# Performance work log

Hardware: AMD Instinct MI355X
Metric: run time of the kernel (lower is better)

Reference implementation:

```python
import jax, jax.numpy as jnp
import numpy as np

DIM = 256
HEADS = 8
DHEAD = 32          # dim // 8
WIN = 128           # attn_window
NBLOCKS = 4
FF_INNER = int(DIM * 4 * 2 / 3)  # 682
SCALE = DHEAD ** -0.5


def layernorm(x, g, b):
    mu = jnp.mean(x, axis=-1, keepdims=True)
    var = jnp.mean((x - mu) ** 2, axis=-1, keepdims=True)
    return (x - mu) * jax.lax.rsqrt(var + 1e-5) * g + b


def look_around(x):
    # x: (b, h, nw, w, d) -> (b, h, nw, 3w, d); prev/current/next window, zero-padded ends
    nw = x.shape[2]
    p = jnp.pad(x, ((0, 0), (0, 0), (1, 1), (0, 0), (0, 0)))
    return jnp.concatenate([p[:, :, i:i + nw] for i in range(3)], axis=3)


def key_mask(mask):
    # mask: (b, n) bool -> (b, nw, 3w) validity of look-around keys
    b, n = mask.shape
    nw = n // WIN
    mb = mask.reshape(b, nw, WIN)
    p = jnp.pad(mb, ((0, 0), (1, 1), (0, 0)), constant_values=False)
    return jnp.concatenate([p[:, i:i + nw] for i in range(3)], axis=-1)


def local_mha(x, kmask, ln_g, ln_b, qkv_w, out_w):
    b, n, _ = x.shape
    nw = n // WIN
    xn = layernorm(x, ln_g, ln_b)
    qkv = jnp.einsum('bnd,ed->bne', xn, qkv_w)           # (b, n, 3*h*dh)
    qkv = qkv.reshape(b, nw, WIN, 3, HEADS, DHEAD)
    q, k, v = [jnp.transpose(qkv[:, :, :, i], (0, 3, 1, 2, 4)) for i in range(3)]  # (b,h,nw,w,dh)
    kk = look_around(k)                                   # (b,h,nw,3w,dh)
    vv = look_around(v)
    sim = jnp.einsum('bhnid,bhnjd->bhnij', q, kk) * SCALE  # (b,h,nw,w,3w)
    neg = -jnp.finfo(sim.dtype).max
    sim = jnp.where(kmask[:, None, :, None, :], sim, neg)
    attn = jax.nn.softmax(sim, axis=-1)
    out = jnp.einsum('bhnij,bhnjd->bhnid', attn, vv)      # (b,h,nw,w,dh)
    out = jnp.transpose(out, (0, 2, 3, 1, 4)).reshape(b, n, HEADS * DHEAD)
    return jnp.einsum('bne,de->bnd', out, out_w)


def geglu_ff(x, ln_g, ln_b, w1, w2):
    xn = layernorm(x, ln_g, ln_b)
    h = jnp.einsum('bnd,ed->bne', xn, w1)                 # (b, n, 2*FF_INNER)
    a, g = jnp.split(h, 2, axis=-1)
    y = a * jax.nn.gelu(g, approximate=False)             # exact GELU like torch
    return jnp.einsum('bne,de->bnd', y, w2)


def setup_inputs() -> dict:
    key = jax.random.key(0)
    ks = jax.random.split(key, 8)
    B, N = 8, 4096
    s = 0.02
    return {
        'x': jax.random.normal(ks[0], (B, N, DIM), dtype=jnp.float32),
        'mask': jnp.ones((B, N), dtype=bool),
        'ln1_g': jnp.ones((NBLOCKS, DIM), jnp.float32),
        'ln1_b': jnp.zeros((NBLOCKS, DIM), jnp.float32),
        'qkv_w': jax.random.normal(ks[1], (NBLOCKS, 3 * HEADS * DHEAD, DIM), jnp.float32) * s,
        'out_w': jax.random.normal(ks[2], (NBLOCKS, DIM, HEADS * DHEAD), jnp.float32) * s,
        'ln2_g': jnp.ones((NBLOCKS, DIM), jnp.float32),
        'ln2_b': jnp.zeros((NBLOCKS, DIM), jnp.float32),
        'ff_w1': jax.random.normal(ks[3], (NBLOCKS, 2 * FF_INNER, DIM), jnp.float32) * s,
        'ff_w2': jax.random.normal(ks[4], (NBLOCKS, DIM, FF_INNER), jnp.float32) * s,
    }


def reference(x, mask, ln1_g, ln1_b, qkv_w, out_w, ln2_g, ln2_b, ff_w1, ff_w2):
    kmask = key_mask(mask)
    for i in range(NBLOCKS):
        x = local_mha(x, kmask, ln1_g[i], ln1_b[i], qkv_w[i], out_w[i]) + x
        x = geglu_ff(x, ln2_g[i], ln2_b[i], ff_w1[i], ff_w2[i]) + x
    return x
```

## Files before the change

### kernel.cpp

```cpp
#include <hip/hip_runtime.h>


#define DIM 256
#define DHEAD 32
#define NWIN 32
#define SEQ 4096
#define TOKENS 32768
#define FFP 704
#define ATT_SCALE_LOG2E 0.25501818642228136f

typedef __attribute__((ext_vector_type(4))) float f32x4;
typedef __attribute__((ext_vector_type(4))) short s16x4;
typedef __attribute__((ext_vector_type(8))) short s16x8;
typedef __attribute__((ext_vector_type(4))) _Float16 f16x4;
typedef __attribute__((ext_vector_type(8))) _Float16 f16x8;

__device__ __forceinline__ short f2bf(float f) {
  unsigned int u = __float_as_uint(f);
  u += 0x7fffu + ((u >> 16) & 1u);
  return (short)(u >> 16);
}

__device__ __forceinline__ float fast_exp2(float x) {
#if __has_builtin(__builtin_amdgcn_exp2f)
  return __builtin_amdgcn_exp2f(x);
#else
  return __expf(x * 0.6931471805599453f);
#endif
}

__device__ __forceinline__ float gelu_as(float g) {
  const float z = fabsf(g) * 0.70710678118654752440f;
#if __has_builtin(__builtin_amdgcn_rcpf)
  const float t = __builtin_amdgcn_rcpf(fmaf(0.3275911f, z, 1.0f));
#else
  const float t = 1.0f / fmaf(0.3275911f, z, 1.0f);
#endif
  const float e = fast_exp2(-z * z * 1.4426950408889634f);
  const float poly = t * fmaf(t, fmaf(t, fmaf(t, fmaf(t, 1.061405429f,
                     -1.453152027f), 1.421413741f), -0.284496736f), 0.254829592f);
  const float erfv = fmaf(-poly, e, 1.0f);
  const float se = (g < 0.0f) ? -erfv : erfv;
  return 0.5f * g * (1.0f + se);
}

__device__ __forceinline__ void gl_lds16(const short* g, short* l) {
  __builtin_amdgcn_global_load_lds(
      (const __attribute__((address_space(1))) void*)g,
      (__attribute__((address_space(3))) void*)l, 16, 0, 0);
}

__device__ __forceinline__ s16x8 fragld(const short* lds, int row, int g) {
  return *(const s16x8*)(lds + row * 64 + ((g ^ (row & 7)) << 3));
}

__global__ void __launch_bounds__(256)
copy_ln(const float* __restrict__ x0, const float* __restrict__ gw,
        const float* __restrict__ bw, float* __restrict__ x, short* __restrict__ xn) {
  const int row = blockIdx.x * 4 + (threadIdx.x >> 6);
  const int lane = threadIdx.x & 63;
  const f32x4 v = *(const f32x4*)(x0 + (size_t)row * DIM + lane * 4);
  *(f32x4*)(x + (size_t)row * DIM + lane * 4) = v;
  float s = v[0] + v[1] + v[2] + v[3];
  float s2 = v[0]*v[0] + v[1]*v[1] + v[2]*v[2] + v[3]*v[3];
#pragma unroll
  for (int off = 32; off > 0; off >>= 1) {
    s  += __shfl_xor(s, off, 64);
    s2 += __shfl_xor(s2, off, 64);
  }
  const float mu = s * (1.0f / DIM);
  const float var = s2 * (1.0f / DIM) - mu * mu;
  const float rstd = rsqrtf(var + 1e-5f);
  const f32x4 gv = *(const f32x4*)(gw + lane * 4);
  const f32x4 bv = *(const f32x4*)(bw + lane * 4);
  s16x4 o;
#pragma unroll
  for (int j = 0; j < 4; ++j) o[j] = f2bf((v[j] - mu) * rstd * gv[j] + bv[j]);
  *(s16x4*)(xn + (size_t)row * DIM + lane * 4) = o;
}

template<int K, bool DO_LN>
__global__ void __launch_bounds__(256, 2)
gemm_res_ln(const short* __restrict__ A, const short* __restrict__ W,
            float* __restrict__ x, const float* __restrict__ lng,
            const float* __restrict__ lnb, short* __restrict__ xn) {
  __shared__ short As[2][64 * 64];
  __shared__ short Bs[2][256 * 64];
  const int tid = threadIdx.x;
  const int lane = tid & 63;
  const int w = tid >> 6;
  const int ln16 = lane & 15;
  const int quad = lane >> 4;
  const int m_blk = blockIdx.x * 64;
  const int n0w = w * 64;
  const int srow = lane >> 3;
  const int swz = (lane & 7) ^ srow;

  const short* sg[10];
  short* dg0[10];
  short* dg1[10];
#pragma unroll
  for (int i = 0; i < 10; ++i) {
    const int grp = w + i * 4;
    if (grp < 8) {
      sg[i] = A + (size_t)(m_blk + grp * 8 + srow) * K + swz * 8;
      dg0[i] = &As[0][grp * 512];
      dg1[i] = &As[1][grp * 512];
    } else {
      const int gb = grp - 8;
      sg[i] = W + (size_t)(gb * 8 + srow) * K + swz * 8;
      dg0[i] = &Bs[0][gb * 512];
      dg1[i] = &Bs[1][gb * 512];
    }
  }

  constexpr int NS = K / 64;
  f32x4 acc[4][4] = {};

#pragma unroll
  for (int i = 0; i < 10; ++i) gl_lds16(sg[i], dg0[i]);
  __syncthreads();

#pragma unroll
  for (int s = 0; s < NS; ++s) {
    if (s + 1 < NS) {
#pragma unroll
      for (int i = 0; i < 10; ++i)
        gl_lds16(sg[i] + (s + 1) * 64, ((s & 1) ? dg0 : dg1)[i]);
    }
    const short* Ac = (s & 1) ? As[1] : As[0];
    const short* Bc = (s & 1) ? Bs[1] : Bs[0];
    s16x8 af[2][4], bf[2][4];
#pragma unroll
    for (int kh = 0; kh < 2; ++kh) {
#pragma unroll
      for (int mt = 0; mt < 4; ++mt)
        af[kh][mt] = fragld(Ac, mt * 16 + ln16, kh * 4 + quad);
#pragma unroll
      for (int nt = 0; nt < 4; ++nt)
        bf[kh][nt] = fragld(Bc, n0w + nt * 16 + ln16, kh * 4 + quad);
    }
#pragma unroll
    for (int kh = 0; kh < 2; ++kh)
#pragma unroll
      for (int mt = 0; mt < 4; ++mt)
#pragma unroll
        for (int nt = 0; nt < 4; ++nt)
          acc[mt][nt] = __builtin_amdgcn_mfma_f32_16x16x32_bf16(af[kh][mt], bf[kh][nt], acc[mt][nt], 0, 0, 0);
    __syncthreads();
  }

#pragma unroll
  for (int mt = 0; mt < 4; ++mt)
#pragma unroll
    for (int nt = 0; nt < 4; ++nt)
#pragma unroll
      for (int r = 0; r < 4; ++r) {
        const size_t idx = (size_t)(m_blk + mt * 16 + quad * 4 + r) * DIM
                           + n0w + nt * 16 + ln16;
        const float v = x[idx] + acc[mt][nt][r];
        acc[mt][nt][r] = v;
        x[idx] = v;
      }

  if (DO_LN) {
    float2* red = (float2*)As[0];
#pragma unroll
    for (int mt = 0; mt < 4; ++mt)
#pragma unroll
      for (int r = 0; r < 4; ++r) {
        float s = 0.f, s2 = 0.f;
#pragma unroll
        for (int nt = 0; nt < 4; ++nt) {
          const float v = acc[mt][nt][r];
          s += v; s2 += v * v;
        }
#pragma unroll
        for (int off = 1; off < 16; off <<= 1) {
          s  += __shfl_xor(s, off, 64);
          s2 += __shfl_xor(s2, off, 64);
        }
        if (ln16 == 0)
          red[(mt * 16 + quad * 4 + r) * 4 + w] = float2{s, s2};
      }
    __syncthreads();

    float gv[4], bv[4];
#pragma unroll
    for (int nt = 0; nt < 4; ++nt) {
      gv[nt] = lng[n0w + nt * 16 + ln16];
      bv[nt] = lnb[n0w + nt * 16 + ln16];
    }
#pragma unroll
    for (int mt = 0; mt < 4; ++mt)
#pragma unroll
      for (int r = 0; r < 4; ++r) {
        const int row = mt * 16 + quad * 4 + r;
        const float2 t0 = red[row * 4 + 0];
        const float2 t1 = red[row * 4 + 1];
        const float2 t2 = red[row * 4 + 2];
        const float2 t3 = red[row * 4 + 3];
        const float s  = (t0.x + t1.x) + (t2.x + t3.x);
        const float s2 = (t0.y + t1.y) + (t2.y + t3.y);
        const float mu = s * (1.0f / DIM);
        const float var = s2 * (1.0f / DIM) - mu * mu;
        const float rstd = rsqrtf(var + 1e-5f);
#pragma unroll
        for (int nt = 0; nt < 4; ++nt)
          xn[(size_t)(m_blk + row) * DIM + n0w + nt * 16 + ln16] =
              f2bf((acc[mt][nt][r] - mu) * rstd * gv[nt] + bv[nt]);
      }
  }
}

__global__ void __launch_bounds__(256, 2)
fused_out_ff1(const short* __restrict__ A, const short* __restrict__ W,
              float* __restrict__ x, const float* __restrict__ lng,
              const float* __restrict__ lnb, const short* __restrict__ wff,
              short* __restrict__ y) {
  __shared__ short As[2][64 * 64];
  __shared__ short Bs[2][256 * 64];
  const int tid = threadIdx.x;
  const int lane = tid & 63;
  const int w = tid >> 6;
  const int ln16 = lane & 15;
  const int quad = lane >> 4;
  const int m_blk = blockIdx.x * 64;
  const int n0w = w * 64;
  const int srow = lane >> 3;
  const int swz = (lane & 7) ^ srow;

  const short* sg[10];
  short* dg0[10];
  short* dg1[10];
#pragma unroll
  for (int i = 0; i < 10; ++i) {
    const int grp = w + i * 4;
    if (grp < 8) {
      sg[i] = A + (size_t)(m_blk + grp * 8 + srow) * DIM + swz * 8;
      dg0[i] = &As[0][grp * 512];
      dg1[i] = &As[1][grp * 512];
    } else {
      const int gb = grp - 8;
      sg[i] = W + (size_t)(gb * 8 + srow) * DIM + swz * 8;
      dg0[i] = &Bs[0][gb * 512];
      dg1[i] = &Bs[1][gb * 512];
    }
  }

  f32x4 acc[4][4] = {};
#pragma unroll
  for (int i = 0; i < 10; ++i) gl_lds16(sg[i], dg0[i]);
  __syncthreads();

#pragma unroll
  for (int s = 0; s < 4; ++s) {
    if (s + 1 < 4) {
#pragma unroll
      for (int i = 0; i < 10; ++i)
        gl_lds16(sg[i] + (s + 1) * 64, ((s & 1) ? dg0 : dg1)[i]);
    }
    const short* Ac = (s & 1) ? As[1] : As[0];
    const short* Bc = (s & 1) ? Bs[1] : Bs[0];
    s16x8 af[2][4], bf[2][4];
#pragma unroll
    for (int kh = 0; kh < 2; ++kh) {
#pragma unroll
      for (int mt = 0; mt < 4; ++mt)
        af[kh][mt] = fragld(Ac, mt * 16 + ln16, kh * 4 + quad);
#pragma unroll
      for (int nt = 0; nt < 4; ++nt)
        bf[kh][nt] = fragld(Bc, n0w + nt * 16 + ln16, kh * 4 + quad);
    }
#pragma unroll
    for (int kh = 0; kh < 2; ++kh)
#pragma unroll
      for (int mt = 0; mt < 4; ++mt)
#pragma unroll
        for (int nt = 0; nt < 4; ++nt)
          acc[mt][nt] = __builtin_amdgcn_mfma_f32_16x16x32_bf16(af[kh][mt], bf[kh][nt], acc[mt][nt], 0, 0, 0);
    __syncthreads();
  }

  short* const xnl = &Bs[0][0];
  short* const Wsl = &Bs[1][0];
  int wbase[4];
#pragma unroll
  for (int i = 0; i < 4; ++i) {
    const int grp = w + i * 4;
    const int half = grp >> 3;
    wbase[i] = (half * FFP + (grp & 7) * 8 + srow) * DIM + swz * 8;
  }
  auto stage2 = [&](int cs2) {
    const int c2 = cs2 >> 2, s2 = cs2 & 3;
    short* db = Wsl + ((cs2 & 1) ? 8192 : 0);
#pragma unroll
    for (int i = 0; i < 4; ++i)
      gl_lds16(wff + wbase[i] + c2 * (64 * DIM) + s2 * 64, db + (w + i * 4) * 512);
  };
  stage2(0);

#pragma unroll
  for (int mt = 0; mt < 4; ++mt)
#pragma unroll
    for (int nt = 0; nt < 4; ++nt)
#pragma unroll
      for (int r = 0; r < 4; ++r) {
        const size_t idx = (size_t)(m_blk + mt * 16 + quad * 4 + r) * DIM
                           + n0w + nt * 16 + ln16;
        const float v = x[idx] + acc[mt][nt][r];
        acc[mt][nt][r] = v;
        x[idx] = v;
      }

  {
    float2* red = (float2*)As[0];
#pragma unroll
    for (int mt = 0; mt < 4; ++mt)
#pragma unroll
      for (int r = 0; r < 4; ++r) {
        float s = 0.f, s2 = 0.f;
#pragma unroll
        for (int nt = 0; nt < 4; ++nt) {
          const float v = acc[mt][nt][r];
          s += v; s2 += v * v;
        }
#pragma unroll
        for (int off = 1; off < 16; off <<= 1) {
          s  += __shfl_xor(s, off, 64);
          s2 += __shfl_xor(s2, off, 64);
        }
        if (ln16 == 0)
          red[(mt * 16 + quad * 4 + r) * 4 + w] = float2{s, s2};
      }
    __syncthreads();

    float gv[4], bv[4];
#pragma unroll
    for (int nt = 0; nt < 4; ++nt) {
      gv[nt] = lng[n0w + nt * 16 + ln16];
      bv[nt] = lnb[n0w + nt * 16 + ln16];
    }
#pragma unroll
    for (int mt = 0; mt < 4; ++mt)
#pragma unroll
      for (int r = 0; r < 4; ++r) {
        const int row = mt * 16 + quad * 4 + r;
        const float2 t0 = red[row * 4 + 0];
        const float2 t1 = red[row * 4 + 1];
        const float2 t2 = red[row * 4 + 2];
        const float2 t3 = red[row * 4 + 3];
        const float s  = (t0.x + t1.x) + (t2.x + t3.x);
        const float s2 = (t0.y + t1.y) + (t2.y + t3.y);
        const float mu = s * (1.0f / DIM);
        const float var = s2 * (1.0f / DIM) - mu * mu;
        const float rstd = rsqrtf(var + 1e-5f);
#pragma unroll
        for (int nt = 0; nt < 4; ++nt) {
          const int colin = nt * 16 + ln16;
          const int pos = ((colin >> 3) ^ (row & 7)) * 8 + (colin & 7);
          xnl[w * 4096 + row * 64 + pos] =
              f2bf((acc[mt][nt][r] - mu) * rstd * gv[nt] + bv[nt]);
        }
      }
  }
  __syncthreads();

  f32x4 aA[4], aG[4];
  for (int cs = 0; cs < 44; ++cs) {
    const int c = cs >> 2, s = cs & 3;
    if (cs + 1 < 44) stage2(cs + 1);
    if (s == 0) {
#pragma unroll
      for (int mt = 0; mt < 4; ++mt) { aA[mt] = f32x4{0.f,0.f,0.f,0.f}; aG[mt] = f32x4{0.f,0.f,0.f,0.f}; }
    }
    const short* Wb = Wsl + ((cs & 1) ? 8192 : 0);
    const short* Xs = xnl + s * 4096;
    s16x8 af[2][4], wa[2], wg[2];
#pragma unroll
    for (int kh = 0; kh < 2; ++kh) {
#pragma unroll
      for (int mt = 0; mt < 4; ++mt)
        af[kh][mt] = fragld(Xs, mt * 16 + ln16, kh * 4 + quad);
      wa[kh] = fragld(Wb, w * 16 + ln16, kh * 4 + quad);
      wg[kh] = fragld(Wb, 64 + w * 16 + ln16, kh * 4 + quad);
    }
#pragma unroll
    for (int kh = 0; kh < 2; ++kh)
#pragma unroll
      for (int mt = 0; mt < 4; ++mt) {
        aA[mt] = __builtin_amdgcn_mfma_f32_16x16x32_bf16(af[kh][mt], wa[kh], aA[mt], 0, 0, 0);
        aG[mt] = __builtin_amdgcn_mfma_f32_16x16x32_bf16(af[kh][mt], wg[kh], aG[mt], 0, 0, 0);
      }
    if (s == 3) {
      const int col = c * 64 + w * 16 + ln16;
#pragma unroll
      for (int mt = 0; mt < 4; ++mt)
#pragma unroll
        for (int r = 0; r < 4; ++r)
          y[(size_t)(m_blk + mt * 16 + quad * 4 + r) * FFP + col] =
              f2bf(aA[mt][r] * gelu_as(aG[mt][r]));
    }
    __syncthreads();
  }
}

__global__ void __launch_bounds__(256)
gemm_qkv(const short* __restrict__ A, const short* __restrict__ W,
         short* __restrict__ qh, short* __restrict__ kh_, _Float16* __restrict__ vp) {
  __shared__ short As[128 * 64];
  __shared__ short Bs[128 * 64];
  const int tid = threadIdx.x;
  const int lane = tid & 63;
  const int w = tid >> 6;
  const int ln16 = lane & 15;
  const int quad = lane >> 4;
  const int m_blk0 = blockIdx.x * 256;
  const int n_blk = blockIdx.y * 128;
  const int m0w = (w & 1) * 64;
  const int n0w = (w >> 1) * 64;
  const int srow = lane >> 3;
  const int swz = (lane & 7) ^ srow;

  int aoff[4];
  const short* bsrc[4];
  short* dst[8];
#pragma unroll
  for (int i = 0; i < 8; ++i) {
    const int grp = w + i * 4;
    if (i < 4) {
      aoff[i] = (grp * 8 + srow) * DIM + swz * 8;
      dst[i] = As + grp * 512;
    } else {
      const int gb = grp - 16;
      bsrc[i - 4] = W + (size_t)(n_blk + gb * 8 + srow) * DIM + swz * 8;
      dst[i] = Bs + gb * 512;
    }
  }

  auto stage = [&](int t2, int s2) {
    const short* At = A + (size_t)(m_blk0 + t2 * 128) * DIM + s2 * 64;
#pragma unroll
    for (int i = 0; i < 4; ++i) gl_lds16(At + aoff[i], dst[i]);
#pragma unroll
    for (int i = 0; i < 4; ++i) gl_lds16(bsrc[i] + s2 * 64, dst[i + 4]);
  };

  stage(0, 0);

#pragma unroll
  for (int t = 0; t < 2; ++t) {
    f32x4 acc[4][4] = {};
#pragma unroll
    for (int s = 0; s < 4; ++s) {
      __syncthreads();
      s16x8 af[2][4], bf[2][4];
#pragma unroll
      for (int kh = 0; kh < 2; ++kh) {
#pragma unroll
        for (int mt = 0; mt < 4; ++mt)
          af[kh][mt] = fragld(As, m0w + mt * 16 + ln16, kh * 4 + quad);
#pragma unroll
        for (int nt = 0; nt < 4; ++nt)
          bf[kh][nt] = fragld(Bs, n0w + nt * 16 + ln16, kh * 4 + quad);
      }
#pragma unroll
      for (int kh = 0; kh < 2; ++kh)
#pragma unroll
        for (int mt = 0; mt < 4; ++mt)
#pragma unroll
          for (int nt = 0; nt < 4; ++nt)
            acc[mt][nt] = __builtin_amdgcn_mfma_f32_16x16x32_bf16(af[kh][mt], bf[kh][nt], acc[mt][nt], 0, 0, 0);
      if (!(t == 1 && s == 3)) {
        __syncthreads();
        if (s == 3) stage(t + 1, 0);
        else        stage(t, s + 1);
      }
    }

#pragma unroll
    for (int mt = 0; mt < 4; ++mt) {
      const int m = m_blk0 + t * 128 + m0w + mt * 16 + quad * 4;
      const int bb = m >> 12;
      const int n = m & 4095;
#pragma unroll
      for (int nt = 0; nt < 4; ++nt) {
        const int f = n_blk + n0w + nt * 16;
        if (f < 512) {
          const int ff = f & 255;
          short* dstp = (f < 256 ? qh : kh_)
                       + ((size_t)(bb * 8 + (ff >> 5)) * SEQ + n) * 32 + (ff & 16) + ln16;
#pragma unroll
          for (int r = 0; r < 4; ++r) dstp[r * 32] = f2bf(acc[mt][nt][r]);
        } else {
          const int ff = f - 512;
          const int h = ff >> 5;
          const int d = (ff & 16) + ln16;
          const int within = n & 31;
          const int pos = (n & ~31) + ((within & 12) << 1) + ((within >> 4) << 2);
          f16x4 o;
#pragma unroll
          for (int r = 0; r < 4; ++r) o[r] = (_Float16)acc[mt][nt][r];
          *(f16x4*)(vp + ((size_t)(bb * 8 + h) * 32 + d) * SEQ + pos) = o;
        }
      }
    }
  }
}

__global__ void __launch_bounds__(256)
attn_kernel(const short* __restrict__ qh, const short* __restrict__ kh,
            const _Float16* __restrict__ vp, short* __restrict__ out) {
  const int blk = blockIdx.x;
  const int lane = threadIdx.x & 63;
  const int wid = threadIdx.x >> 6;
  const int ln16 = lane & 15;
  const int quad = lane >> 4;

  const int w = (blk & 15) * 2 + (wid >> 1);
  const int h = (blk >> 4) & 7;
  const int b = blk >> 7;
  const int plane = b * 8 + h;
  const int tok0 = w * 128 + (wid & 1) * 64;
  const int ktok = w * 128 - 128;
  const int c0 = (w == 0) ? 4 : 0;
  const int c1 = (w == NWIN - 1) ? 8 : 12;

  const short* qp = qh + ((size_t)plane * SEQ + tok0) * 32;
  s16x8 qf[4];
#pragma unroll
  for (int qi = 0; qi < 4; ++qi)
    qf[qi] = *(const s16x8*)(qp + (qi * 16 + ln16) * 32 + quad * 8);

  const short* kp = kh + ((size_t)plane * SEQ + ktok) * 32;
  const _Float16* vb = vp + ((size_t)plane * 32 + ln16) * SEQ + ktok;

  float lsum[4] = {0.f, 0.f, 0.f, 0.f};
  f32x4 ot[4][2] = {};

  s16x8 kc0 = *(const s16x8*)(kp + (c0 * 32 + ln16) * 32 + quad * 8);
  s16x8 kc1 = *(const s16x8*)(kp + (c0 * 32 + 16 + ln16) * 32 + quad * 8);
  f16x8 vc0 = *(const f16x8*)(vb + c0 * 32 + quad * 8);
  f16x8 vc1 = *(const f16x8*)(vb + (size_t)16 * SEQ + c0 * 32 + quad * 8);

  for (int c = c0; c < c1; ++c) {
    const int cn = (c + 1 < c1) ? c + 1 : c;
    s16x8 kn0 = *(const s16x8*)(kp + (cn * 32 + ln16) * 32 + quad * 8);
    s16x8 kn1 = *(const s16x8*)(kp + (cn * 32 + 16 + ln16) * 32 + quad * 8);
    f16x8 vn0 = *(const f16x8*)(vb + cn * 32 + quad * 8);
    f16x8 vn1 = *(const f16x8*)(vb + (size_t)16 * SEQ + cn * 32 + quad * 8);

    const f16x4 v00 = __builtin_shufflevector(vc0, vc0, 0, 1, 2, 3);
    const f16x4 v10 = __builtin_shufflevector(vc0, vc0, 4, 5, 6, 7);
    const f16x4 v01 = __builtin_shufflevector(vc1, vc1, 0, 1, 2, 3);
    const f16x4 v11 = __builtin_shufflevector(vc1, vc1, 4, 5, 6, 7);

#pragma unroll
    for (int qi = 0; qi < 4; ++qi) {
      const f32x4 z = {0.f, 0.f, 0.f, 0.f};
      f32x4 st0 = __builtin_amdgcn_mfma_f32_16x16x32_bf16(kc0, qf[qi], z, 0, 0, 0);
      f32x4 st1 = __builtin_amdgcn_mfma_f32_16x16x32_bf16(kc1, qf[qi], z, 0, 0, 0);
      float p[8];
#pragma unroll
      for (int r = 0; r < 4; ++r) {
        p[r]     = fast_exp2(st0[r] * ATT_SCALE_LOG2E);
        p[4 + r] = fast_exp2(st1[r] * ATT_SCALE_LOG2E);
      }
      lsum[qi] += ((p[0] + p[1]) + (p[2] + p[3])) + ((p[4] + p[5]) + (p[6] + p[7]));
      f16x4 pa, pb;
#pragma unroll
      for (int r = 0; r < 4; ++r) { pa[r] = (_Float16)p[r]; pb[r] = (_Float16)p[4 + r]; }
      ot[qi][0] = __builtin_amdgcn_mfma_f32_16x16x16f16(pa, v00, ot[qi][0], 0, 0, 0);
      ot[qi][1] = __builtin_amdgcn_mfma_f32_16x16x16f16(pa, v01, ot[qi][1], 0, 0, 0);
      ot[qi][0] = __builtin_amdgcn_mfma_f32_16x16x16f16(pb, v10, ot[qi][0], 0, 0, 0);
      ot[qi][1] = __builtin_amdgcn_mfma_f32_16x16x16f16(pb, v11, ot[qi][1], 0, 0, 0);
    }
    kc0 = kn0; kc1 = kn1; vc0 = vn0; vc1 = vn1;
  }

#pragma unroll
  for (int qi = 0; qi < 4; ++qi) {
    float l = lsum[qi];
    l += __shfl_xor(l, 16, 64);
    l += __shfl_xor(l, 32, 64);
    const float inv = 1.0f / l;
#pragma unroll
    for (int dt = 0; dt < 2; ++dt)
#pragma unroll
      for (int r = 0; r < 4; ++r)
        out[(size_t)(b * SEQ + tok0 + qi * 16 + quad * 4 + r) * DIM
            + h * DHEAD + dt * 16 + ln16] = f2bf(ot[qi][dt][r] * inv);
  }
}

__global__ void cvt_all(const float* __restrict__ qkv_w, const float* __restrict__ out_w,
                        const float* __restrict__ ff_w1, const float* __restrict__ ff_w2,
                        short* __restrict__ wqkv, short* __restrict__ wout,
                        short* __restrict__ wff1, short* __restrict__ wff2) {
  int i = blockIdx.x * 256 + threadIdx.x;
  if (i < 786432) { wqkv[i] = f2bf(qkv_w[i]); return; }
  i -= 786432;
  if (i < 262144) { wout[i] = f2bf(out_w[i]); return; }
  i -= 262144;
  if (i < 1441792) {
    const int c = i & 255;
    const int rl = i >> 8;
    const int l = rl / 1408;
    const int r = rl - l * 1408;
    const int half = r / FFP;
    const int rr = r - half * FFP;
    const float v = (rr < 682) ? ff_w1[((size_t)(l * 1364 + half * 682 + rr)) * 256 + c] : 0.0f;
    wff1[i] = f2bf(v);
    return;
  }
  i -= 1441792;
  if (i < 720896) {
    const int c = i % FFP;
    const int t = i / FFP;
    const float v = (c < 682) ? ff_w2[(size_t)t * 682 + c] : 0.0f;
    wff2[i] = f2bf(v);
  }
}

extern "C" void kernel_launch(void* const* d_in, const int* in_sizes, int n_in,
                              void* d_out, int out_size, void* d_ws, size_t ws_size,
                              hipStream_t stream) {
  const float* x0    = (const float*)d_in[0];
  const float* ln1_g = (const float*)d_in[2];
  const float* ln1_b = (const float*)d_in[3];
  const float* qkv_w = (const float*)d_in[4];
  const float* out_w = (const float*)d_in[5];
  const float* ln2_g = (const float*)d_in[6];
  const float* ln2_b = (const float*)d_in[7];
  const float* ff_w1 = (const float*)d_in[8];
  const float* ff_w2 = (const float*)d_in[9];
  float* x = (float*)d_out;

  char* ws = (char*)d_ws;
  short* wqkv = (short*)(ws);
  short* wout = (short*)(ws + 1572864);
  short* wff1 = (short*)(ws + 2097152);
  short* wff2 = (short*)(ws + 4980736);
  short* xn   = (short*)(ws + 6422528);
  short*    qhb = (short*)(ws + 23199744);
  short*    khb = (short*)(ws + 23199744 + 16777216);
  _Float16* vpb = (_Float16*)(ws + 23199744 + 33554432);
  short*    yb  = (short*)(ws + 23199744);

  copy_ln<<<8192, 256, 0, stream>>>(x0, ln1_g, ln1_b, x, xn);
  cvt_all<<<12544, 256, 0, stream>>>(qkv_w, out_w, ff_w1, ff_w2, wqkv, wout, wff1, wff2);

  for (int l = 0; l < 4; ++l) {
    gemm_qkv<<<dim3(128, 6), 256, 0, stream>>>(
        xn, wqkv + (size_t)l * 768 * DIM, qhb, khb, vpb);
    attn_kernel<<<1024, 256, 0, stream>>>(qhb, khb, vpb, xn);
    fused_out_ff1<<<512, 256, 0, stream>>>(
        xn, wout + (size_t)l * DIM * DIM, x,
        ln2_g + l * DIM, ln2_b + l * DIM,
        wff1 + (size_t)l * 2 * FFP * DIM, yb);
    if (l < 3)
      gemm_res_ln<FFP, true><<<512, 256, 0, stream>>>(
          yb, wff2 + (size_t)l * DIM * FFP, x,
          ln1_g + (l + 1) * DIM, ln1_b + (l + 1) * DIM, xn);
    else
      gemm_res_ln<FFP, false><<<512, 256, 0, stream>>>(
          yb, wff2 + (size_t)l * DIM * FFP, x, nullptr, nullptr, nullptr);
  }
}
```

Measured before the change: 718.6 us.

## Load weight fragments directly from global memory instead of staging through LDS

In gemm_res_ln and fused_out_ff1, the B (weight) operand is no longer copied into shared memory. Each lane now reads its MFMA fragments straight from global memory, relying on L1/L2 caching because every block reuses the same small weight matrix. The FF1 loop also drops its LDS double-buffered weight staging and the per-chunk barriers, and the 2-blocks-per-CU launch bound is removed. This frees a lot of LDS and removes sync overhead, at the cost of uncoalesced global loads on the critical path whose latency is no longer hidden by a prefetch.

```diff
diff --git a/kernel.cpp b/kernel.cpp
--- a/kernel.cpp
+++ b/kernel.cpp
@@ -80,12 +80,11 @@
 }
 
 template<int K, bool DO_LN>
-__global__ void __launch_bounds__(256, 2)
+__global__ void __launch_bounds__(256)
 gemm_res_ln(const short* __restrict__ A, const short* __restrict__ W,
             float* __restrict__ x, const float* __restrict__ lng,
             const float* __restrict__ lnb, short* __restrict__ xn) {
   __shared__ short As[2][64 * 64];
-  __shared__ short Bs[2][256 * 64];
   const int tid = threadIdx.x;
   const int lane = tid & 63;
   const int w = tid >> 6;
@@ -96,50 +95,48 @@
   const int srow = lane >> 3;
   const int swz = (lane & 7) ^ srow;
 
-  const short* sg[10];
-  short* dg0[10];
-  short* dg1[10];
-#pragma unroll
-  for (int i = 0; i < 10; ++i) {
+  const short* sg[2];
+  short* dg0[2];
+  short* dg1[2];
+#pragma unroll
+  for (int i = 0; i < 2; ++i) {
     const int grp = w + i * 4;
-    if (grp < 8) {
-      sg[i] = A + (size_t)(m_blk + grp * 8 + srow) * K + swz * 8;
-      dg0[i] = &As[0][grp * 512];
-      dg1[i] = &As[1][grp * 512];
-    } else {
-      const int gb = grp - 8;
-      sg[i] = W + (size_t)(gb * 8 + srow) * K + swz * 8;
-      dg0[i] = &Bs[0][gb * 512];
-      dg1[i] = &Bs[1][gb * 512];
-    }
-  }
+    sg[i] = A + (size_t)(m_blk + grp * 8 + srow) * K + swz * 8;
+    dg0[i] = &As[0][grp * 512];
+    dg1[i] = &As[1][grp * 512];
+  }
+
+  const short* wr[4];
+#pragma unroll
+  for (int nt = 0; nt < 4; ++nt)
+    wr[nt] = W + (size_t)(n0w + nt * 16 + ln16) * K + quad * 8;
 
   constexpr int NS = K / 64;
   f32x4 acc[4][4] = {};
 
 #pragma unroll
-  for (int i = 0; i < 10; ++i) gl_lds16(sg[i], dg0[i]);
+  for (int i = 0; i < 2; ++i) gl_lds16(sg[i], dg0[i]);
   __syncthreads();
 
 #pragma unroll
   for (int s = 0; s < NS; ++s) {
     if (s + 1 < NS) {
 #pragma unroll
-      for (int i = 0; i < 10; ++i)
+      for (int i = 0; i < 2; ++i)
         gl_lds16(sg[i] + (s + 1) * 64, ((s & 1) ? dg0 : dg1)[i]);
     }
     const short* Ac = (s & 1) ? As[1] : As[0];
-    const short* Bc = (s & 1) ? Bs[1] : Bs[0];
     s16x8 af[2][4], bf[2][4];
 #pragma unroll
-    for (int kh = 0; kh < 2; ++kh) {
+    for (int nt = 0; nt < 4; ++nt) {
+      bf[0][nt] = *(const s16x8*)(wr[nt] + s * 64);
+      bf[1][nt] = *(const s16x8*)(wr[nt] + s * 64 + 32);
+    }
+#pragma unroll
+    for (int kh = 0; kh < 2; ++kh)
 #pragma unroll
       for (int mt = 0; mt < 4; ++mt)
         af[kh][mt] = fragld(Ac, mt * 16 + ln16, kh * 4 + quad);
-#pragma unroll
-      for (int nt = 0; nt < 4; ++nt)
-        bf[kh][nt] = fragld(Bc, n0w + nt * 16 + ln16, kh * 4 + quad);
-    }
 #pragma unroll
     for (int kh = 0; kh < 2; ++kh)
 #pragma unroll
@@ -213,13 +210,13 @@
   }
 }
 
-__global__ void __launch_bounds__(256, 2)
+__global__ void __launch_bounds__(256)
 fused_out_ff1(const short* __restrict__ A, const short* __restrict__ W,
               float* __restrict__ x, const float* __restrict__ lng,
               const float* __restrict__ lnb, const short* __restrict__ wff,
               short* __restrict__ y) {
   __shared__ short As[2][64 * 64];
-  __shared__ short Bs[2][256 * 64];
+  __shared__ short xnl[64 * 256];
   const int tid = threadIdx.x;
   const int lane = tid & 63;
   const int w = tid >> 6;
@@ -230,48 +227,45 @@
   const int srow = lane >> 3;
   const int swz = (lane & 7) ^ srow;
 
-  const short* sg[10];
-  short* dg0[10];
-  short* dg1[10];
-#pragma unroll
-  for (int i = 0; i < 10; ++i) {
+  const short* sg[2];
+  short* dg0[2];
+  short* dg1[2];
+#pragma unroll
+  for (int i = 0; i < 2; ++i) {
     const int grp = w + i * 4;
-    if (grp < 8) {
-      sg[i] = A + (size_t)(m_blk + grp * 8 + srow) * DIM + swz * 8;
-      dg0[i] = &As[0][grp * 512];
-      dg1[i] = &As[1][grp * 512];
-    } else {
-      const int gb = grp - 8;
-      sg[i] = W + (size_t)(gb * 8 + srow) * DIM + swz * 8;
-      dg0[i] = &Bs[0][gb * 512];
-      dg1[i] = &Bs[1][gb * 512];
-    }
-  }
+    sg[i] = A + (size_t)(m_blk + grp * 8 + srow) * DIM + swz * 8;
+    dg0[i] = &As[0][grp * 512];
+    dg1[i] = &As[1][grp * 512];
+  }
+  const short* wr[4];
+#pragma unroll
+  for (int nt = 0; nt < 4; ++nt)
+    wr[nt] = W + (size_t)(n0w + nt * 16 + ln16) * DIM + quad * 8;
 
   f32x4 acc[4][4] = {};
 #pragma unroll
-  for (int i = 0; i < 10; ++i) gl_lds16(sg[i], dg0[i]);
+  for (int i = 0; i < 2; ++i) gl_lds16(sg[i], dg0[i]);
   __syncthreads();
 
 #pragma unroll
   for (int s = 0; s < 4; ++s) {
     if (s + 1 < 4) {
 #pragma unroll
-      for (int i = 0; i < 10; ++i)
+      for (int i = 0; i < 2; ++i)
         gl_lds16(sg[i] + (s + 1) * 64, ((s & 1) ? dg0 : dg1)[i]);
     }
     const short* Ac = (s & 1) ? As[1] : As[0];
-    const short* Bc = (s & 1) ? Bs[1] : Bs[0];
     s16x8 af[2][4], bf[2][4];
 #pragma unroll
-    for (int kh = 0; kh < 2; ++kh) {
+    for (int nt = 0; nt < 4; ++nt) {
+      bf[0][nt] = *(const s16x8*)(wr[nt] + s * 64);
+      bf[1][nt] = *(const s16x8*)(wr[nt] + s * 64 + 32);
+    }
+#pragma unroll
+    for (int kh = 0; kh < 2; ++kh)
 #pragma unroll
       for (int mt = 0; mt < 4; ++mt)
         af[kh][mt] = fragld(Ac, mt * 16 + ln16, kh * 4 + quad);
-#pragma unroll
-      for (int nt = 0; nt < 4; ++nt)
-        bf[kh][nt] = fragld(Bc, n0w + nt * 16 + ln16, kh * 4 + quad);
-    }
 #pragma unroll
     for (int kh = 0; kh < 2; ++kh)
 #pragma unroll
@@ -281,24 +275,6 @@
           acc[mt][nt] = __builtin_amdgcn_mfma_f32_16x16x32_bf16(af[kh][mt], bf[kh][nt], acc[mt][nt], 0, 0, 0);
     __syncthreads();
   }
-
-  short* const xnl = &Bs[0][0];
-  short* const Wsl = &Bs[1][0];
-  int wbase[4];
-#pragma unroll
-  for (int i = 0; i < 4; ++i) {
-    const int grp = w + i * 4;
-    const int half = grp >> 3;
-    wbase[i] = (half * FFP + (grp & 7) * 8 + srow) * DIM + swz * 8;
-  }
-  auto stage2 = [&](int cs2) {
-    const int c2 = cs2 >> 2, s2 = cs2 & 3;
-    short* db = Wsl + ((cs2 & 1) ? 8192 : 0);
-#pragma unroll
-    for (int i = 0; i < 4; ++i)
-      gl_lds16(wff + wbase[i] + c2 * (64 * DIM) + s2 * 64, db + (w + i * 4) * 512);
-  };
-  stage2(0);
 
 #pragma unroll
   for (int mt = 0; mt < 4; ++mt)
@@ -366,42 +342,40 @@
   }
   __syncthreads();
 
-  f32x4 aA[4], aG[4];
-  for (int cs = 0; cs < 44; ++cs) {
-    const int c = cs >> 2, s = cs & 3;
-    if (cs + 1 < 44) stage2(cs + 1);
-    if (s == 0) {
-#pragma unroll
-      for (int mt = 0; mt < 4; ++mt) { aA[mt] = f32x4{0.f,0.f,0.f,0.f}; aG[mt] = f32x4{0.f,0.f,0.f,0.f}; }
-    }
-    const short* Wb = Wsl + ((cs & 1) ? 8192 : 0);
-    const short* Xs = xnl + s * 4096;
-    s16x8 af[2][4], wa[2], wg[2];
-#pragma unroll
-    for (int kh = 0; kh < 2; ++kh) {
-#pragma unroll
-      for (int mt = 0; mt < 4; ++mt)
-        af[kh][mt] = fragld(Xs, mt * 16 + ln16, kh * 4 + quad);
-      wa[kh] = fragld(Wb, w * 16 + ln16, kh * 4 + quad);
-      wg[kh] = fragld(Wb, 64 + w * 16 + ln16, kh * 4 + quad);
-    }
-#pragma unroll
-    for (int kh = 0; kh < 2; ++kh)
-#pragma unroll
-      for (int mt = 0; mt < 4; ++mt) {
-        aA[mt] = __builtin_amdgcn_mfma_f32_16x16x32_bf16(af[kh][mt], wa[kh], aA[mt], 0, 0, 0);
-        aG[mt] = __builtin_amdgcn_mfma_f32_16x16x32_bf16(af[kh][mt], wg[kh], aG[mt], 0, 0, 0);
-      }
-    if (s == 3) {
-      const int col = c * 64 + w * 16 + ln16;
-#pragma unroll
-      for (int mt = 0; mt < 4; ++mt)
-#pragma unroll
-        for (int r = 0; r < 4; ++r)
-          y[(size_t)(m_blk + mt * 16 + quad * 4 + r) * FFP + col] =
-              f2bf(aA[mt][r] * gelu_as(aG[mt][r]));
-    }
-    __syncthreads();
+  const short* wfa = wff + (size_t)(w * 16 + ln16) * DIM + quad * 8;
+  const short* wfg = wff + (size_t)(FFP + w * 16 + ln16) * DIM + quad * 8;
+  for (int c = 0; c < 11; ++c) {
+    f32x4 aA[4] = {}, aG[4] = {};
+    const size_t crow = (size_t)c * 64 * DIM;
+#pragma unroll
+    for (int s = 0; s < 4; ++s) {
+      s16x8 wa[2], wg[2];
+      wa[0] = *(const s16x8*)(wfa + crow + s * 64);
+      wa[1] = *(const s16x8*)(wfa + crow + s * 64 + 32);
+      wg[0] = *(const s16x8*)(wfg + crow + s * 64);
+      wg[1] = *(const s16x8*)(wfg + crow + s * 64 + 32);
+      const short* Xs = xnl + s * 4096;
+      s16x8 af[2][4];
+#pragma unroll
+      for (int kh = 0; kh < 2; ++kh)
+#pragma unroll
+        for (int mt = 0; mt < 4; ++mt)
+          af[kh][mt] = fragld(Xs, mt * 16 + ln16, kh * 4 + quad);
+#pragma unroll
+      for (int kh = 0; kh < 2; ++kh)
+#pragma unroll
+        for (int mt = 0; mt < 4; ++mt) {
+          aA[mt] = __builtin_amdgcn_mfma_f32_16x16x32_bf16(af[kh][mt], wa[kh], aA[mt], 0, 0, 0);
+          aG[mt] = __builtin_amdgcn_mfma_f32_16x16x32_bf16(af[kh][mt], wg[kh], aG[mt], 0, 0, 0);
+        }
+    }
+    const int col = c * 64 + w * 16 + ln16;
+#pragma unroll
+    for (int mt = 0; mt < 4; ++mt)
+#pragma unroll
+      for (int r = 0; r < 4; ++r)
+        y[(size_t)(m_blk + mt * 16 + quad * 4 + r) * FFP + col] =
+            f2bf(aA[mt][r] * gelu_as(aG[mt][r]));
   }
 }
 
```

After: 812.6 us. 13.1% more time.
